# Optimization experiments

Measured on AMD Instinct MI355X. Metric: run time of the kernel, lower is better.

The kernel has to match this reference:

```python
import jax, jax.numpy as jnp
import numpy as np

I, J, B, H = 256, 256, 64, 1024
NHID, NCLS = 1024, 3


def setup_inputs() -> dict:
    key = jax.random.key(0)
    ks = jax.random.split(key, 12)
    inp = {
        "P_enc": jax.random.normal(ks[0], (I, B, H), jnp.float32),
        "H_enc": jax.random.normal(ks[1], (J, B, H), jnp.float32),
        "P_emb": jax.random.normal(ks[2], (I, B, H), jnp.float32),
        "H_emb": jax.random.normal(ks[3], (J, B, H), jnp.float32),
        "prem_mask": jax.random.bernoulli(ks[4], 0.15, (I, B)),
        "hypo_mask": jax.random.bernoulli(ks[5], 0.15, (J, B)),
        # compare MLP: Linear(2H, NHID) -> ReLU -> Linear(NHID, NHID) -> ReLU
        "cW1": jax.random.normal(ks[6], (2 * H, NHID), jnp.float32) * 0.02,
        "cb1": jnp.zeros((NHID,), jnp.float32),
        "cW2": jax.random.normal(ks[7], (NHID, NHID), jnp.float32) * 0.02,
        "cb2": jnp.zeros((NHID,), jnp.float32),
        # agg MLP: Linear(2*NHID, NHID) -> ReLU -> Linear(NHID, NCLS)
        "aW1": jax.random.normal(ks[8], (2 * NHID, NHID), jnp.float32) * 0.02,
        "ab1": jnp.zeros((NHID,), jnp.float32),
        "aW2": jax.random.normal(ks[9], (NHID, NCLS), jnp.float32) * 0.02,
        "ab2": jnp.zeros((NCLS,), jnp.float32),
    }
    return inp


def reference(P_enc, H_enc, P_emb, H_emb, prem_mask, hypo_mask,
              cW1, cb1, cW2, cb2, aW1, ab1, aW2, ab2):
    # Dropout is identity at inference.
    def compare(x):
        h = jax.nn.relu(x @ cW1 + cb1)
        return jax.nn.relu(h @ cW2 + cb2)

    # S[b,i,j] = <P_enc[i,b,:], H_enc[j,b,:]>
    S = jnp.einsum('ibh,jbh->bij', P_enc, H_enc)

    # Premise-side masking on rows i, softmax over premise positions (axis=1)
    S_m = jnp.where(prem_mask.T[:, :, None], -jnp.inf, S)  # [b,i,j]
    P_attn = jax.nn.softmax(S_m, axis=1)
    H_ctx = jnp.einsum('bij,ibh->jbh', P_attn, P_emb)      # [j,b,h]
    H_ctx = jnp.where(hypo_mask[:, :, None], 0.0, H_ctx)
    H_comp = compare(jnp.concatenate([H_emb, H_ctx], axis=-1))  # [j,b,nhid]

    # Hypothesis-side: transpose of the UNMASKED scores
    St = jnp.swapaxes(S, 1, 2)                              # [b,j,i]
    St = jnp.where(hypo_mask.T[:, :, None], -jnp.inf, St)
    H_attn = jax.nn.softmax(St, axis=1)
    P_ctx = jnp.einsum('bji,jbh->ibh', H_attn, H_emb)       # [i,b,h]
    P_ctx = jnp.where(prem_mask[:, :, None], 0.0, P_ctx)
    P_comp = compare(jnp.concatenate([P_emb, P_ctx], axis=-1))  # [i,b,nhid]

    pool = jnp.concatenate([H_comp.sum(axis=0), P_comp.sum(axis=0)], axis=-1)  # [b, 2*nhid]
    out = jax.nn.relu(pool @ aW1 + ab1) @ aW2 + ab2          # [b, ncls]
    return out
```

## Files before the change

### kernel.cpp

```cpp
#include <hip/hip_runtime.h>
#include <cstdint>
#include <cstddef>

typedef unsigned short ushort_t;
typedef unsigned char uchar_t;
typedef __attribute__((ext_vector_type(4))) float f4;
typedef __attribute__((ext_vector_type(4))) unsigned int u4;
typedef __attribute__((ext_vector_type(2))) unsigned int u2;

#define DEVI static __device__ __forceinline__

DEVI ushort_t f2bf(float x) {
  union { float f; unsigned int u; } v; v.f = x;
  unsigned int r = v.u + 0x7fffu + ((v.u >> 16) & 1u);
  return (ushort_t)(r >> 16);
}
DEVI float bf2f(ushort_t b) {
  union { unsigned int u; float f; } v; v.u = ((unsigned int)b) << 16;
  return v.f;
}
DEVI unsigned pk2(ushort_t a, ushort_t b) { return (unsigned)a | ((unsigned)b << 16); }

DEVI void mfma16(f4& c, u4 a, u4 b) {
  asm("v_mfma_f32_16x16x32_bf16 %0, %1, %2, %0" : "+v"(c) : "v"(a), "v"(b));
}

constexpr int LDR = 40;

#if defined(__has_builtin)
#if __has_builtin(__builtin_amdgcn_global_load_lds)
#define HAS_GLD 1
#endif
#endif
#ifndef HAS_GLD
#define HAS_GLD 0
#endif

#if HAS_GLD
typedef const __attribute__((address_space(1))) unsigned int* gas1_t;
typedef __attribute__((address_space(3))) unsigned int* las3_t;
DEVI void gld16(const void* g, void* l) {
  __builtin_amdgcn_global_load_lds((gas1_t)g, (las3_t)l, 16, 0, 0);
}
#endif

DEVI void stage_tile(const ushort_t* __restrict__ src, int srcStride, int k0,
                     ushort_t* lT, int t) {
#if HAS_GLD
  int w = t >> 6, lane = t & 63;
#pragma unroll
  for (int c = 0; c < 2; ++c) {
    int row = c * 64 + w * 16 + (lane >> 2);
    const ushort_t* g = src + (size_t)row * srcStride + k0 + (lane & 3) * 8;
    gld16(g, lT + (c * 64 + w * 16) * 32);
  }
#else
  int row = t >> 1, kp = (t & 1) << 4;
  const ushort_t* g = src + (size_t)row * srcStride + k0 + kp;
  *(u4*)(lT + row * 32 + kp) = *(const u4*)g;
  *(u4*)(lT + row * 32 + kp + 8) = *(const u4*)(g + 8);
#endif
}

DEVI void compute16(const ushort_t* lA, const ushort_t* lB, f4 acc[4][4],
                    int wr, int wc, int fr, int fg) {
  u4 af[4], bfv[4];
#pragma unroll
  for (int m = 0; m < 4; ++m) af[m] = *(const u4*)(lA + (wr + m * 16 + fr) * 32 + (fg << 3));
#pragma unroll
  for (int n = 0; n < 4; ++n) bfv[n] = *(const u4*)(lB + (wc + n * 16 + fr) * 32 + (fg << 3));
#pragma unroll
  for (int m = 0; m < 4; ++m)
#pragma unroll
    for (int n = 0; n < 4; ++n) mfma16(acc[m][n], af[m], bfv[n]);
}

__global__ __launch_bounds__(256) void prep_masks_kernel(
    const uchar_t* __restrict__ prem, const uchar_t* __restrict__ hypo,
    uchar_t* __restrict__ premT, uchar_t* __restrict__ hypoT) {
  __shared__ int flagP, flagH;
  int t = threadIdx.x;
  if (t == 0) { flagP = 0; flagH = 0; }
  __syncthreads();
  int locP = 0, locH = 0;
  for (int i = t; i < 16384; i += 256) {
    if (i & 3) { locP |= prem[i]; locH |= hypo[i]; }
  }
  if (locP) atomicOr(&flagP, 1);
  if (locH) atomicOr(&flagH, 1);
  __syncthreads();
  bool p8 = flagP != 0, h8 = flagH != 0;
  for (int i = t; i < 16384; i += 256) {
    int p = i >> 6, b = i & 63;
    premT[b * 256 + p] = p8 ? prem[i] : prem[i * 4];
    hypoT[b * 256 + p] = h8 ? hypo[i] : hypo[i * 4];
  }
}

__global__ __launch_bounds__(256) void transpose_w_kernel(
    const float* __restrict__ Win, ushort_t* __restrict__ Thi,
    ushort_t* __restrict__ Tlo, int N, int K) {
  __shared__ float tl[64][65];
  int k0 = blockIdx.x * 64, n0 = blockIdx.y * 64;
  int t = threadIdx.x;
#pragma unroll
  for (int it = 0; it < 16; ++it) {
    int idx = t + it * 256;
    int k = idx >> 6, n = idx & 63;
    tl[n][k] = Win[(size_t)(k0 + k) * N + n0 + n];
  }
  __syncthreads();
#pragma unroll
  for (int it = 0; it < 16; ++it) {
    int idx = t + it * 256;
    int n = idx >> 6, k = idx & 63;
    float x = tl[n][k];
    ushort_t h = f2bf(x);
    Thi[(size_t)(n0 + n) * K + k0 + k] = h;
    if (Tlo) Tlo[(size_t)(n0 + n) * K + k0 + k] = f2bf(x - bf2f(h));
  }
}

__global__ __launch_bounds__(256) void gemm_s_kernel(
    const float* __restrict__ Penc, const float* __restrict__ Henc,
    float* __restrict__ S) {
  __shared__ ushort_t lAh[64 * LDR], lAl[64 * LDR], lBh[64 * LDR], lBl[64 * LDR];
  const int t = threadIdx.x;
  const int b = blockIdx.z;
  const int i0 = blockIdx.x * 64, j0 = blockIdx.y * 64;
  const int lda = 64 * 1024;
  const float* Ab = Penc + (size_t)i0 * lda + (size_t)b * 1024;
  const float* Bb = Henc + (size_t)j0 * lda + (size_t)b * 1024;
  const int lane = t & 63, wave = t >> 6;
  const int wr = (wave >> 1) << 5, wc = (wave & 1) << 5;
  const int fr = lane & 15, fg = lane >> 4;

  f4 acc[2][2];
#pragma unroll
  for (int m = 0; m < 2; ++m)
#pragma unroll
    for (int n = 0; n < 2; ++n) acc[m][n] = f4{0.f, 0.f, 0.f, 0.f};

  const int row = t >> 2, kp = (t & 3) << 3;
  for (int k0 = 0; k0 < 1024; k0 += 32) {
    {
      const float* p = Ab + (size_t)row * lda + k0 + kp;
      f4 x0 = *(const f4*)p, x1 = *(const f4*)(p + 4);
      ushort_t hh[8], ll[8];
#pragma unroll
      for (int q = 0; q < 4; ++q) {
        ushort_t h0 = f2bf(x0[q]); hh[q] = h0; ll[q] = f2bf(x0[q] - bf2f(h0));
        ushort_t h1 = f2bf(x1[q]); hh[4 + q] = h1; ll[4 + q] = f2bf(x1[q] - bf2f(h1));
      }
      *(u4*)(lAh + row * LDR + kp) = u4{ pk2(hh[0], hh[1]), pk2(hh[2], hh[3]), pk2(hh[4], hh[5]), pk2(hh[6], hh[7]) };
      *(u4*)(lAl + row * LDR + kp) = u4{ pk2(ll[0], ll[1]), pk2(ll[2], ll[3]), pk2(ll[4], ll[5]), pk2(ll[6], ll[7]) };
    }
    {
      const float* p = Bb + (size_t)row * lda + k0 + kp;
      f4 x0 = *(const f4*)p, x1 = *(const f4*)(p + 4);
      ushort_t hh[8], ll[8];
#pragma unroll
      for (int q = 0; q < 4; ++q) {
        ushort_t h0 = f2bf(x0[q]); hh[q] = h0; ll[q] = f2bf(x0[q] - bf2f(h0));
        ushort_t h1 = f2bf(x1[q]); hh[4 + q] = h1; ll[4 + q] = f2bf(x1[q] - bf2f(h1));
      }
      *(u4*)(lBh + row * LDR + kp) = u4{ pk2(hh[0], hh[1]), pk2(hh[2], hh[3]), pk2(hh[4], hh[5]), pk2(hh[6], hh[7]) };
      *(u4*)(lBl + row * LDR + kp) = u4{ pk2(ll[0], ll[1]), pk2(ll[2], ll[3]), pk2(ll[4], ll[5]), pk2(ll[6], ll[7]) };
    }
    __syncthreads();
    u4 ah[2], al[2], bh[2], bl[2];
#pragma unroll
    for (int m = 0; m < 2; ++m) {
      int off = (wr + m * 16 + fr) * LDR + (fg << 3);
      ah[m] = *(const u4*)(lAh + off);
      al[m] = *(const u4*)(lAl + off);
    }
#pragma unroll
    for (int n = 0; n < 2; ++n) {
      int off = (wc + n * 16 + fr) * LDR + (fg << 3);
      bh[n] = *(const u4*)(lBh + off);
      bl[n] = *(const u4*)(lBl + off);
    }
#pragma unroll
    for (int m = 0; m < 2; ++m)
#pragma unroll
      for (int n = 0; n < 2; ++n) {
        mfma16(acc[m][n], ah[m], bh[n]);
        mfma16(acc[m][n], ah[m], bl[n]);
        mfma16(acc[m][n], al[m], bh[n]);
      }
    __syncthreads();
  }

  float* Sb = S + (size_t)b * 65536;
#pragma unroll
  for (int m = 0; m < 2; ++m)
#pragma unroll
    for (int n = 0; n < 2; ++n)
#pragma unroll
      for (int r = 0; r < 4; ++r) {
        int rrow = i0 + wr + m * 16 + fg * 4 + r;
        int col = j0 + wc + n * 16 + fr;
        Sb[(size_t)rrow * 256 + col] = acc[m][n][r];
      }
}

__global__ __launch_bounds__(256) void softmax_rows_kernel(
    const float* __restrict__ S, const uchar_t* __restrict__ hypoT,
    ushort_t* __restrict__ W) {
  int r = blockIdx.x * 4 + (threadIdx.x >> 6);
  int lane = threadIdx.x & 63;
  int b = r >> 8;
  const float* row = S + (size_t)r * 256;
  f4 x = *(const f4*)(row + lane * 4);
  const uchar_t* mp = hypoT + b * 256 + lane * 4;
  float v0 = mp[0] ? -1e30f : x[0];
  float v1 = mp[1] ? -1e30f : x[1];
  float v2 = mp[2] ? -1e30f : x[2];
  float v3 = mp[3] ? -1e30f : x[3];
  float m = fmaxf(fmaxf(v0, v1), fmaxf(v2, v3));
#pragma unroll
  for (int off = 32; off > 0; off >>= 1) m = fmaxf(m, __shfl_xor(m, off));
  float e0 = expf(v0 - m), e1 = expf(v1 - m), e2 = expf(v2 - m), e3 = expf(v3 - m);
  float s = e0 + e1 + e2 + e3;
#pragma unroll
  for (int off = 32; off > 0; off >>= 1) s += __shfl_xor(s, off);
  float rinv = 1.0f / s;
  ushort_t w0 = f2bf(e0 * rinv), w1 = f2bf(e1 * rinv), w2 = f2bf(e2 * rinv), w3 = f2bf(e3 * rinv);
  *(u2*)(W + (size_t)r * 256 + lane * 4) = u2{ pk2(w0, w1), pk2(w2, w3) };
}

__global__ __launch_bounds__(256) void softmax_cols_kernel(
    const float* __restrict__ S, const uchar_t* __restrict__ premT,
    ushort_t* __restrict__ V) {
  __shared__ float tl[32][257];
  __shared__ float pm[8][32], ps[8][32], mfin[32], rs[32];
  int t = threadIdx.x;
  int jl = t & 31, ig = t >> 5;
  int b = blockIdx.y, j0 = blockIdx.x * 32;
  const float* Sb = S + (size_t)b * 65536;
  const uchar_t* pmsk = premT + b * 256;
  for (int i = ig; i < 256; i += 8)
    tl[jl][i] = pmsk[i] ? -1e30f : Sb[(size_t)i * 256 + j0 + jl];
  __syncthreads();
  float m = -3e30f;
#pragma unroll 8
  for (int ii = 0; ii < 32; ++ii) m = fmaxf(m, tl[jl][ig * 32 + ii]);
  float s = 0.f;
#pragma unroll 8
  for (int ii = 0; ii < 32; ++ii) s += expf(tl[jl][ig * 32 + ii] - m);
  pm[ig][jl] = m; ps[ig][jl] = s;
  __syncthreads();
  if (t < 32) {
    float M = pm[0][t];
#pragma unroll
    for (int g = 1; g < 8; ++g) M = fmaxf(M, pm[g][t]);
    float ss = 0.f;
#pragma unroll
    for (int g = 0; g < 8; ++g) ss += ps[g][t] * expf(pm[g][t] - M);
    mfin[t] = M; rs[t] = 1.0f / ss;
  }
  __syncthreads();
  for (int j2 = 0; j2 < 32; ++j2) {
    float val = expf(tl[j2][t] - mfin[j2]) * rs[j2];
    V[((size_t)b * 256 + j0 + j2) * 256 + t] = f2bf(val);
  }
}

__global__ __launch_bounds__(256) void transpose_pos_h_kernel(
    const float* __restrict__ E, ushort_t* __restrict__ T) {
  __shared__ ushort_t tl[64][65];
  int i0 = blockIdx.x * 64, h0 = blockIdx.y * 64, b = blockIdx.z;
  int t = threadIdx.x;
#pragma unroll
  for (int it = 0; it < 16; ++it) {
    int idx = t + it * 256;
    int i = idx >> 6, h = idx & 63;
    tl[h][i] = f2bf(E[((size_t)(i0 + i) * 64 + b) * 1024 + h0 + h]);
  }
  __syncthreads();
#pragma unroll
  for (int it = 0; it < 16; ++it) {
    int idx = t + it * 256;
    int h = idx >> 6, i = idx & 63;
    T[((size_t)b * 1024 + h0 + h) * 256 + i0 + i] = tl[h][i];
  }
}

__global__ __launch_bounds__(256) void gemm_ctx_kernel(
    const ushort_t* __restrict__ Attn, const ushort_t* __restrict__ T,
    const uchar_t* __restrict__ maskT, ushort_t* __restrict__ Xc) {
  __shared__ ushort_t lA[128 * 32], lB[128 * 32];
  int t = threadIdx.x;
  int b = blockIdx.z;
  int m0 = blockIdx.x * 128, n0 = blockIdx.y * 128;
  const ushort_t* A = Attn + (size_t)b * 65536 + (size_t)m0 * 256;
  const ushort_t* B = T + (size_t)b * 262144 + (size_t)n0 * 256;
  int lane = t & 63, wave = t >> 6;
  int wr = (wave >> 1) << 6, wc = (wave & 1) << 6;
  int fr = lane & 15, fg = lane >> 4;
  f4 acc[4][4];
#pragma unroll
  for (int m = 0; m < 4; ++m)
#pragma unroll
    for (int n = 0; n < 4; ++n) acc[m][n] = f4{0.f, 0.f, 0.f, 0.f};
  for (int k0 = 0; k0 < 256; k0 += 32) {
    stage_tile(A, 256, k0, lA, t);
    stage_tile(B, 256, k0, lB, t);
    __syncthreads();
    compute16(lA, lB, acc, wr, wc, fr, fg);
    __syncthreads();
  }
#pragma unroll
  for (int m = 0; m < 4; ++m)
#pragma unroll
    for (int n = 0; n < 4; ++n)
#pragma unroll
      for (int r = 0; r < 4; ++r) {
        int gm = m0 + wr + m * 16 + fg * 4 + r;
        int gn = n0 + wc + n * 16 + fr;
        float v = maskT[b * 256 + gm] ? 0.f : acc[m][n][r];
        Xc[((size_t)gm * 64 + b) * 1024 + gn] = f2bf(v);
      }
}

__global__ __launch_bounds__(256) void gemm_mlp_kernel(
    const float* __restrict__ Ef, const ushort_t* __restrict__ Actx,
    const ushort_t* __restrict__ W, int ldw, const float* __restrict__ bias,
    ushort_t* __restrict__ C, int Kb) {
  __shared__ ushort_t lA[128 * 32], lB[128 * 32];
  int t = threadIdx.x;
  int m0 = blockIdx.x * 128, n0 = blockIdx.y * 128;
  int lane = t & 63, wave = t >> 6;
  int wr = (wave >> 1) << 6, wc = (wave & 1) << 6;
  int fr = lane & 15, fg = lane >> 4;
  f4 acc[4][4];
#pragma unroll
  for (int m = 0; m < 4; ++m)
#pragma unroll
    for (int n = 0; n < 4; ++n) acc[m][n] = f4{0.f, 0.f, 0.f, 0.f};

  const ushort_t* Wn = W + (size_t)n0 * ldw;
  if (Ef) {
    int row = t >> 1, kp = (t & 1) << 4;
    for (int k0 = 0; k0 < 1024; k0 += 32) {
      const float* p = Ef + (size_t)(m0 + row) * 1024 + k0 + kp;
      f4 x0 = *(const f4*)p, x1 = *(const f4*)(p + 4);
      f4 x2 = *(const f4*)(p + 8), x3 = *(const f4*)(p + 12);
      ushort_t hh[16];
#pragma unroll
      for (int q = 0; q < 4; ++q) {
        hh[q] = f2bf(x0[q]); hh[4 + q] = f2bf(x1[q]);
        hh[8 + q] = f2bf(x2[q]); hh[12 + q] = f2bf(x3[q]);
      }
      *(u4*)(lA + row * 32 + kp) =
          u4{ pk2(hh[0], hh[1]), pk2(hh[2], hh[3]), pk2(hh[4], hh[5]), pk2(hh[6], hh[7]) };
      *(u4*)(lA + row * 32 + kp + 8) =
          u4{ pk2(hh[8], hh[9]), pk2(hh[10], hh[11]), pk2(hh[12], hh[13]), pk2(hh[14], hh[15]) };
      stage_tile(Wn, ldw, k0, lB, t);
      __syncthreads();
      compute16(lA, lB, acc, wr, wc, fr, fg);
      __syncthreads();
    }
  }
  const ushort_t* Abase = Actx + (size_t)m0 * Kb;
  const int wkoff = Ef ? 1024 : 0;
  for (int k0 = 0; k0 < Kb; k0 += 32) {
    stage_tile(Abase, Kb, k0, lA, t);
    stage_tile(Wn, ldw, wkoff + k0, lB, t);
    __syncthreads();
    compute16(lA, lB, acc, wr, wc, fr, fg);
    __syncthreads();
  }

#pragma unroll
  for (int m = 0; m < 4; ++m)
#pragma unroll
    for (int n = 0; n < 4; ++n)
#pragma unroll
      for (int r = 0; r < 4; ++r) {
        int gm = m0 + wr + m * 16 + fg * 4 + r;
        int gn = n0 + wc + n * 16 + fr;
        float v = acc[m][n][r] + bias[gn];
        v = v > 0.f ? v : 0.f;
        C[(size_t)gm * 1024 + gn] = f2bf(v);
      }
}

__global__ __launch_bounds__(256) void pool_partial_kernel(
    const ushort_t* __restrict__ H2, float* __restrict__ partial, int coff) {
  int jc = blockIdx.x, b = blockIdx.y, t = threadIdx.x;
  float a0 = 0.f, a1 = 0.f, a2 = 0.f, a3 = 0.f;
  for (int j = jc * 32; j < jc * 32 + 32; ++j) {
    u2 v = *(const u2*)(H2 + ((size_t)(j * 64 + b)) * 1024 + t * 4);
    a0 += bf2f((ushort_t)(v[0] & 0xffff));
    a1 += bf2f((ushort_t)(v[0] >> 16));
    a2 += bf2f((ushort_t)(v[1] & 0xffff));
    a3 += bf2f((ushort_t)(v[1] >> 16));
  }
  *(f4*)(partial + ((size_t)(jc * 64 + b)) * 2048 + coff + t * 4) = f4{a0, a1, a2, a3};
}

__global__ __launch_bounds__(256) void pool_final_kernel(
    const float* __restrict__ partial, ushort_t* __restrict__ ph,
    ushort_t* __restrict__ pl) {
  int idx = blockIdx.x * 256 + threadIdx.x;
  int b = idx >> 11, k = idx & 2047;
  float s = 0.f;
#pragma unroll
  for (int jc = 0; jc < 8; ++jc) s += partial[((size_t)(jc * 64 + b)) * 2048 + k];
  ushort_t h = f2bf(s);
  ph[idx] = h;
  pl[idx] = f2bf(s - bf2f(h));
}

__global__ __launch_bounds__(256) void gemm_agg1_kernel(
    const ushort_t* __restrict__ Ph, const ushort_t* __restrict__ Pl,
    const ushort_t* __restrict__ Wh, const ushort_t* __restrict__ Wl,
    const float* __restrict__ bias, float* __restrict__ z) {
  __shared__ ushort_t lAh[64 * LDR], lAl[64 * LDR], lBh[128 * LDR], lBl[128 * LDR];
  int t = threadIdx.x;
  int n0 = blockIdx.x * 128;
  int lane = t & 63, wave = t >> 6;
  int wc = wave * 32;
  int fr = lane & 15, fg = lane >> 4;
  f4 acc[4][2];
#pragma unroll
  for (int m = 0; m < 4; ++m)
#pragma unroll
    for (int n = 0; n < 2; ++n) acc[m][n] = f4{0.f, 0.f, 0.f, 0.f};

  for (int k0 = 0; k0 < 2048; k0 += 32) {
    __syncthreads();
    {
      int row = t >> 2, kp = (t & 3) << 3;
      *(u4*)(lAh + row * LDR + kp) = *(const u4*)(Ph + (size_t)row * 2048 + k0 + kp);
      *(u4*)(lAl + row * LDR + kp) = *(const u4*)(Pl + (size_t)row * 2048 + k0 + kp);
    }
#pragma unroll
    for (int c = 0; c < 2; ++c) {
      int ch = t + (c << 8);
      int row = ch >> 2, kp = (ch & 3) << 3;
      *(u4*)(lBh + row * LDR + kp) = *(const u4*)(Wh + (size_t)(n0 + row) * 2048 + k0 + kp);
      *(u4*)(lBl + row * LDR + kp) = *(const u4*)(Wl + (size_t)(n0 + row) * 2048 + k0 + kp);
    }
    __syncthreads();
    u4 ah[4], al[4], bh[2], bl[2];
#pragma unroll
    for (int m = 0; m < 4; ++m) {
      int off = (m * 16 + fr) * LDR + (fg << 3);
      ah[m] = *(const u4*)(lAh + off);
      al[m] = *(const u4*)(lAl + off);
    }
#pragma unroll
    for (int n = 0; n < 2; ++n) {
      int off = (wc + n * 16 + fr) * LDR + (fg << 3);
      bh[n] = *(const u4*)(lBh + off);
      bl[n] = *(const u4*)(lBl + off);
    }
#pragma unroll
    for (int m = 0; m < 4; ++m)
#pragma unroll
      for (int n = 0; n < 2; ++n) {
        mfma16(acc[m][n], ah[m], bh[n]);
        mfma16(acc[m][n], ah[m], bl[n]);
        mfma16(acc[m][n], al[m], bh[n]);
      }
  }
#pragma unroll
  for (int m = 0; m < 4; ++m)
#pragma unroll
    for (int n = 0; n < 2; ++n)
#pragma unroll
      for (int r = 0; r < 4; ++r) {
        int row = m * 16 + fg * 4 + r;
        int col = n0 + wc + n * 16 + fr;
        float v = acc[m][n][r] + bias[col];
        z[row * 1024 + col] = v > 0.f ? v : 0.f;
      }
}

__global__ __launch_bounds__(64) void agg2_kernel(
    const float* __restrict__ z, const float* __restrict__ aW2,
    const float* __restrict__ ab2, float* __restrict__ out) {
  int b = blockIdx.x, lane = threadIdx.x;
  float a0 = 0.f, a1 = 0.f, a2 = 0.f;
  for (int k = lane; k < 1024; k += 64) {
    float zv = z[b * 1024 + k];
    a0 += zv * aW2[k * 3 + 0];
    a1 += zv * aW2[k * 3 + 1];
    a2 += zv * aW2[k * 3 + 2];
  }
#pragma unroll
  for (int off = 32; off > 0; off >>= 1) {
    a0 += __shfl_xor(a0, off);
    a1 += __shfl_xor(a1, off);
    a2 += __shfl_xor(a2, off);
  }
  if (lane == 0) {
    out[b * 3 + 0] = a0 + ab2[0];
    out[b * 3 + 1] = a1 + ab2[1];
    out[b * 3 + 2] = a2 + ab2[2];
  }
}

extern "C" void kernel_launch(void* const* d_in, const int* in_sizes, int n_in,
                              void* d_out, int out_size, void* d_ws, size_t ws_size,
                              hipStream_t stream) {
  const float* P_enc = (const float*)d_in[0];
  const float* H_enc = (const float*)d_in[1];
  const float* P_emb = (const float*)d_in[2];
  const float* H_emb = (const float*)d_in[3];
  const uchar_t* prem = (const uchar_t*)d_in[4];
  const uchar_t* hypo = (const uchar_t*)d_in[5];
  const float* cW1 = (const float*)d_in[6];
  const float* cb1 = (const float*)d_in[7];
  const float* cW2 = (const float*)d_in[8];
  const float* cb2 = (const float*)d_in[9];
  const float* aW1 = (const float*)d_in[10];
  const float* ab1 = (const float*)d_in[11];
  const float* aW2 = (const float*)d_in[12];
  const float* ab2 = (const float*)d_in[13];

  char* w = (char*)d_ws;
  auto alloc = [&](size_t bytes) { char* p = w; w += bytes; return p; };
  float* S        = (float*)alloc(16777216);
  ushort_t* Wsm   = (ushort_t*)alloc(8388608);
  ushort_t* Vsm   = (ushort_t*)alloc(8388608);
  ushort_t* T     = (ushort_t*)alloc(33554432);
  ushort_t* Xc    = (ushort_t*)alloc(33554432);
  ushort_t* H1    = (ushort_t*)alloc(33554432);
  ushort_t* H2    = (ushort_t*)alloc(33554432);
  ushort_t* cW1T  = (ushort_t*)alloc(4194304);
  ushort_t* cW2T  = (ushort_t*)alloc(2097152);
  ushort_t* aW1Th = (ushort_t*)alloc(4194304);
  ushort_t* aW1Tl = (ushort_t*)alloc(4194304);
  float* partial  = (float*)alloc(4194304);
  ushort_t* poolh = (ushort_t*)alloc(262144);
  ushort_t* pooll = (ushort_t*)alloc(262144);
  float* z        = (float*)alloc(262144);
  uchar_t* premT  = (uchar_t*)alloc(16384);
  uchar_t* hypoT  = (uchar_t*)alloc(16384);

  prep_masks_kernel<<<1, 256, 0, stream>>>(prem, hypo, premT, hypoT);
  transpose_w_kernel<<<dim3(32, 16), 256, 0, stream>>>(cW1, cW1T, (ushort_t*)nullptr, 1024, 2048);
  transpose_w_kernel<<<dim3(16, 16), 256, 0, stream>>>(cW2, cW2T, (ushort_t*)nullptr, 1024, 1024);
  transpose_w_kernel<<<dim3(32, 16), 256, 0, stream>>>(aW1, aW1Th, aW1Tl, 1024, 2048);

  gemm_s_kernel<<<dim3(4, 4, 64), 256, 0, stream>>>(P_enc, H_enc, S);
  softmax_rows_kernel<<<4096, 256, 0, stream>>>(S, hypoT, Wsm);
  softmax_cols_kernel<<<dim3(8, 64), 256, 0, stream>>>(S, premT, Vsm);

  transpose_pos_h_kernel<<<dim3(4, 16, 64), 256, 0, stream>>>(P_emb, T);
  gemm_ctx_kernel<<<dim3(2, 8, 64), 256, 0, stream>>>(Vsm, T, hypoT, Xc);
  gemm_mlp_kernel<<<dim3(128, 8), 256, 0, stream>>>(H_emb, Xc, cW1T, 2048, cb1, H1, 1024);
  gemm_mlp_kernel<<<dim3(128, 8), 256, 0, stream>>>(nullptr, H1, cW2T, 1024, cb2, H2, 1024);
  pool_partial_kernel<<<dim3(8, 64), 256, 0, stream>>>(H2, partial, 0);

  transpose_pos_h_kernel<<<dim3(4, 16, 64), 256, 0, stream>>>(H_emb, T);
  gemm_ctx_kernel<<<dim3(2, 8, 64), 256, 0, stream>>>(Wsm, T, premT, Xc);
  gemm_mlp_kernel<<<dim3(128, 8), 256, 0, stream>>>(P_emb, Xc, cW1T, 2048, cb1, H1, 1024);
  gemm_mlp_kernel<<<dim3(128, 8), 256, 0, stream>>>(nullptr, H1, cW2T, 1024, cb2, H2, 1024);
  pool_partial_kernel<<<dim3(8, 64), 256, 0, stream>>>(H2, partial, 1024);

  pool_final_kernel<<<512, 256, 0, stream>>>(partial, poolh, pooll);
  gemm_agg1_kernel<<<8, 256, 0, stream>>>(poolh, pooll, aW1Th, aW1Tl, ab1, z);
  agg2_kernel<<<64, 64, 0, stream>>>(z, aW2, ab2, (float*)d_out);
}
```

Measured before the change: 640.2 us.

## Double-buffer LDS in GEMMs and pre-cast embeddings into concatenated bf16 buffer

Adds a double-buffered shared-memory main loop used by the context and MLP GEMMs, so the next K tile is staged while the current one is computed, with one barrier per step instead of two. The fp32-to-bf16 conversion of the embedding half is moved out of the MLP GEMM into a separate cast kernel. That kernel writes into the left half of a 2048-wide concatenated X buffer, and the context GEMM writes the right half. The first MLP GEMM then becomes a uniform bf16 GEMM over K=2048. This costs twice the LDS per block, which may lower occupancy, plus an extra kernel launch and extra memory traffic for the bf16 copy.

```diff
diff --git a/kernel.cpp b/kernel.cpp
--- a/kernel.cpp
+++ b/kernel.cpp
@@ -287,10 +287,43 @@
   }
 }
 
+__global__ __launch_bounds__(256) void cast_half_kernel(
+    const float* __restrict__ E, ushort_t* __restrict__ X) {
+  size_t idx = (size_t)blockIdx.x * 256 + threadIdx.x;
+  size_t r = idx >> 7;
+  int h8 = ((int)idx & 127) << 3;
+  const f4* p = (const f4*)(E + r * 1024 + h8);
+  f4 a = p[0], c = p[1];
+  ushort_t hh[8];
+#pragma unroll
+  for (int q = 0; q < 4; ++q) { hh[q] = f2bf(a[q]); hh[4 + q] = f2bf(c[q]); }
+  *(u4*)(X + r * 2048 + h8) =
+      u4{ pk2(hh[0], hh[1]), pk2(hh[2], hh[3]), pk2(hh[4], hh[5]), pk2(hh[6], hh[7]) };
+}
+
+DEVI void gemm_2ph(const ushort_t* __restrict__ A, int lda,
+                   const ushort_t* __restrict__ B, int ldb, int K,
+                   ushort_t (*lA)[128 * 32], ushort_t (*lB)[128 * 32],
+                   f4 acc[4][4], int t, int wr, int wc, int fr, int fg) {
+  stage_tile(A, lda, 0, lA[0], t);
+  stage_tile(B, ldb, 0, lB[0], t);
+  __syncthreads();
+  int nt = K >> 5;
+  for (int tt = 0; tt < nt; ++tt) {
+    int cur = tt & 1;
+    if (tt + 1 < nt) {
+      stage_tile(A, lda, (tt + 1) << 5, lA[cur ^ 1], t);
+      stage_tile(B, ldb, (tt + 1) << 5, lB[cur ^ 1], t);
+    }
+    compute16(lA[cur], lB[cur], acc, wr, wc, fr, fg);
+    __syncthreads();
+  }
+}
+
 __global__ __launch_bounds__(256) void gemm_ctx_kernel(
     const ushort_t* __restrict__ Attn, const ushort_t* __restrict__ T,
-    const uchar_t* __restrict__ maskT, ushort_t* __restrict__ Xc) {
-  __shared__ ushort_t lA[128 * 32], lB[128 * 32];
+    const uchar_t* __restrict__ maskT, ushort_t* __restrict__ X) {
+  __shared__ ushort_t lA[2][128 * 32], lB[2][128 * 32];
   int t = threadIdx.x;
   int b = blockIdx.z;
   int m0 = blockIdx.x * 128, n0 = blockIdx.y * 128;
@@ -304,13 +337,7 @@
   for (int m = 0; m < 4; ++m)
 #pragma unroll
     for (int n = 0; n < 4; ++n) acc[m][n] = f4{0.f, 0.f, 0.f, 0.f};
-  for (int k0 = 0; k0 < 256; k0 += 32) {
-    stage_tile(A, 256, k0, lA, t);
-    stage_tile(B, 256, k0, lB, t);
-    __syncthreads();
-    compute16(lA, lB, acc, wr, wc, fr, fg);
-    __syncthreads();
-  }
+  gemm_2ph(A, 256, B, 256, 256, lA, lB, acc, t, wr, wc, fr, fg);
 #pragma unroll
   for (int m = 0; m < 4; ++m)
 #pragma unroll
@@ -320,15 +347,14 @@
         int gm = m0 + wr + m * 16 + fg * 4 + r;
         int gn = n0 + wc + n * 16 + fr;
         float v = maskT[b * 256 + gm] ? 0.f : acc[m][n][r];
-        Xc[((size_t)gm * 64 + b) * 1024 + gn] = f2bf(v);
+        X[((size_t)gm * 64 + b) * 2048 + 1024 + gn] = f2bf(v);
       }
 }
 
 __global__ __launch_bounds__(256) void gemm_mlp_kernel(
-    const float* __restrict__ Ef, const ushort_t* __restrict__ Actx,
-    const ushort_t* __restrict__ W, int ldw, const float* __restrict__ bias,
-    ushort_t* __restrict__ C, int Kb) {
-  __shared__ ushort_t lA[128 * 32], lB[128 * 32];
+    const ushort_t* __restrict__ A, int lda, const ushort_t* __restrict__ W,
+    int ldw, const float* __restrict__ bias, ushort_t* __restrict__ C, int K) {
+  __shared__ ushort_t lA[2][128 * 32], lB[2][128 * 32];
   int t = threadIdx.x;
   int m0 = blockIdx.x * 128, n0 = blockIdx.y * 128;
   int lane = t & 63, wave = t >> 6;
@@ -339,40 +365,8 @@
   for (int m = 0; m < 4; ++m)
 #pragma unroll
     for (int n = 0; n < 4; ++n) acc[m][n] = f4{0.f, 0.f, 0.f, 0.f};
-
-  const ushort_t* Wn = W + (size_t)n0 * ldw;
-  if (Ef) {
-    int row = t >> 1, kp = (t & 1) << 4;
-    for (int k0 = 0; k0 < 1024; k0 += 32) {
-      const float* p = Ef + (size_t)(m0 + row) * 1024 + k0 + kp;
-      f4 x0 = *(const f4*)p, x1 = *(const f4*)(p + 4);
-      f4 x2 = *(const f4*)(p + 8), x3 = *(const f4*)(p + 12);
-      ushort_t hh[16];
-#pragma unroll
-      for (int q = 0; q < 4; ++q) {
-        hh[q] = f2bf(x0[q]); hh[4 + q] = f2bf(x1[q]);
-        hh[8 + q] = f2bf(x2[q]); hh[12 + q] = f2bf(x3[q]);
-      }
-      *(u4*)(lA + row * 32 + kp) =
-          u4{ pk2(hh[0], hh[1]), pk2(hh[2], hh[3]), pk2(hh[4], hh[5]), pk2(hh[6], hh[7]) };
-      *(u4*)(lA + row * 32 + kp + 8) =
-          u4{ pk2(hh[8], hh[9]), pk2(hh[10], hh[11]), pk2(hh[12], hh[13]), pk2(hh[14], hh[15]) };
-      stage_tile(Wn, ldw, k0, lB, t);
-      __syncthreads();
-      compute16(lA, lB, acc, wr, wc, fr, fg);
-      __syncthreads();
-    }
-  }
-  const ushort_t* Abase = Actx + (size_t)m0 * Kb;
-  const int wkoff = Ef ? 1024 : 0;
-  for (int k0 = 0; k0 < Kb; k0 += 32) {
-    stage_tile(Abase, Kb, k0, lA, t);
-    stage_tile(Wn, ldw, wkoff + k0, lB, t);
-    __syncthreads();
-    compute16(lA, lB, acc, wr, wc, fr, fg);
-    __syncthreads();
-  }
-
+  gemm_2ph(A + (size_t)m0 * lda, lda, W + (size_t)n0 * ldw, ldw, K,
+           lA, lB, acc, t, wr, wc, fr, fg);
 #pragma unroll
   for (int m = 0; m < 4; ++m)
 #pragma unroll
@@ -528,7 +522,7 @@
   ushort_t* Wsm   = (ushort_t*)alloc(8388608);
   ushort_t* Vsm   = (ushort_t*)alloc(8388608);
   ushort_t* T     = (ushort_t*)alloc(33554432);
-  ushort_t* Xc    = (ushort_t*)alloc(33554432);
+  ushort_t* X     = (ushort_t*)alloc(67108864);
   ushort_t* H1    = (ushort_t*)alloc(33554432);
   ushort_t* H2    = (ushort_t*)alloc(33554432);
   ushort_t* cW1T  = (ushort_t*)alloc(4194304);
@@ -552,15 +546,17 @@
   softmax_cols_kernel<<<dim3(8, 64), 256, 0, stream>>>(S, premT, Vsm);
 
   transpose_pos_h_kernel<<<dim3(4, 16, 64), 256, 0, stream>>>(P_emb, T);
-  gemm_ctx_kernel<<<dim3(2, 8, 64), 256, 0, stream>>>(Vsm, T, hypoT, Xc);
-  gemm_mlp_kernel<<<dim3(128, 8), 256, 0, stream>>>(H_emb, Xc, cW1T, 2048, cb1, H1, 1024);
-  gemm_mlp_kernel<<<dim3(128, 8), 256, 0, stream>>>(nullptr, H1, cW2T, 1024, cb2, H2, 1024);
+  cast_half_kernel<<<8192, 256, 0, stream>>>(H_emb, X);
+  gemm_ctx_kernel<<<dim3(2, 8, 64), 256, 0, stream>>>(Vsm, T, hypoT, X);
+  gemm_mlp_kernel<<<dim3(128, 8), 256, 0, stream>>>(X, 2048, cW1T, 2048, cb1, H1, 2048);
+  gemm_mlp_kernel<<<dim3(128, 8), 256, 0, stream>>>(H1, 1024, cW2T, 1024, cb2, H2, 1024);
   pool_partial_kernel<<<dim3(8, 64), 256, 0, stream>>>(H2, partial, 0);
 
   transpose_pos_h_kernel<<<dim3(4, 16, 64), 256, 0, stream>>>(H_emb, T);
-  gemm_ctx_kernel<<<dim3(2, 8, 64), 256, 0, stream>>>(Wsm, T, premT, Xc);
-  gemm_mlp_kernel<<<dim3(128, 8), 256, 0, stream>>>(P_emb, Xc, cW1T, 2048, cb1, H1, 1024);
-  gemm_mlp_kernel<<<dim3(128, 8), 256, 0, stream>>>(nullptr, H1, cW2T, 1024, cb2, H2, 1024);
+  cast_half_kernel<<<8192, 256, 0, stream>>>(P_emb, X);
+  gemm_ctx_kernel<<<dim3(2, 8, 64), 256, 0, stream>>>(Wsm, T, premT, X);
+  gemm_mlp_kernel<<<dim3(128, 8), 256, 0, stream>>>(X, 2048, cW1T, 2048, cb1, H1, 2048);
+  gemm_mlp_kernel<<<dim3(128, 8), 256, 0, stream>>>(H1, 1024, cW2T, 1024, cb2, H2, 1024);
   pool_partial_kernel<<<dim3(8, 64), 256, 0, stream>>>(H2, partial, 1024);
 
   pool_final_kernel<<<512, 256, 0, stream>>>(partial, poolh, pooll);
```

New measurement: 654.4 us. 2.2% more time.
